# Kernel optimization log

Measured on AMD Instinct MI355X. Metric: run time of the kernel, lower is better.

## Reference

```python
import jax, jax.numpy as jnp
import numpy as np

N = 50000      # nodes
E = 800000     # edges
IN = 64        # in_feats
HID = 4        # hidden_size
OUT = 64       # out_feats
COORS = 3
EPS = 1e-07
NEG_SLOPE = 0.01  # F.leaky_relu default


def setup_inputs() -> dict:
    key = jax.random.key(0)
    ks = jax.random.split(key, 10)
    feat = jax.random.normal(ks[0], (N, IN), dtype=jnp.float32)
    pos = jax.random.normal(ks[1], (N, COORS), dtype=jnp.float32)
    src = jax.random.randint(ks[2], (E,), 0, N, dtype=jnp.int32)
    dst = jax.random.randint(ks[3], (E,), 0, N, dtype=jnp.int32)
    W_self = jax.random.normal(ks[4], (OUT, IN), dtype=jnp.float32) * 0.1
    W_sp = jax.random.normal(ks[5], (HID * IN, COORS), dtype=jnp.float32) * 0.3
    b_sp = jax.random.normal(ks[6], (HID * IN,), dtype=jnp.float32) * 0.05
    W_neigh = jax.random.normal(ks[7], (OUT, HID * IN), dtype=jnp.float32) * 0.05
    b_neigh = jax.random.normal(ks[8], (OUT,), dtype=jnp.float32) * 0.05
    bias = jnp.zeros((OUT,), dtype=jnp.float32)
    return {"feat": feat, "pos": pos, "src": src, "dst": dst,
            "W_self": W_self, "W_sp": W_sp, "b_sp": b_sp,
            "W_neigh": W_neigh, "b_neigh": b_neigh, "bias": bias}


def reference(feat, pos, src, dst, W_self, W_sp, b_sp, W_neigh, b_neigh, bias):
    # per-edge spatial weighting
    rel = pos[dst] - pos[src]                                   # [E, 3]
    scal = jnp.linalg.norm(rel, axis=1, keepdims=True) + EPS    # [E, 1]
    ws = (rel + 1.0) / scal                                     # [E, 3]
    s = jax.nn.leaky_relu(ws @ W_sp.T + b_sp, NEG_SLOPE)        # [E, HID*IN]
    # modulate gathered src features: reshape(E, IN, HID) * h_src[:, :, None]
    msg = (s.reshape(E, IN, HID) * feat[src][:, :, None]).reshape(E, IN * HID)
    # mean aggregation per destination node (zero for isolated nodes)
    neigh_sum = jax.ops.segment_sum(msg, dst, num_segments=N)   # [N, IN*HID]
    cnt = jax.ops.segment_sum(jnp.ones((E,), feat.dtype), dst, num_segments=N)
    neigh_h = neigh_sum / jnp.maximum(cnt, 1.0)[:, None]
    # output projections
    h_neigh = neigh_h @ W_neigh.T + b_neigh                     # [N, OUT]
    rst = feat @ W_self.T + h_neigh + bias                      # [N, OUT]
    return rst
```

## Files before the change

kernel.cpp:

```cpp
#include <hip/hip_runtime.h>
#include <math.h>

#define N_NODES 50000
#define N_EDGES 800000
#define EPS 1e-7f
#define NEG_SLOPE 0.01f

#define SUBCAP 16
#define GSLOTS 64
#define RSTRIDE 72
#define CSTRIDE 16
#define ZPAD 50000u
#define FEAT_BLOCKS (N_NODES * 64 / 4 / 256)
#define EDGE_BLOCKS4 782
#define ACC_STRIDE 264

typedef __attribute__((ext_vector_type(8))) short short8;
typedef __attribute__((ext_vector_type(4))) float f32x4;

__device__ __forceinline__ unsigned bf16_rne(float x) {
    unsigned u = __float_as_uint(x);
    u += 0x7fffu + ((u >> 16) & 1u);
    return u >> 16;
}
__device__ __forceinline__ unsigned pack_bf16(float a, float b) {
    return bf16_rne(a) | (bf16_rne(b) << 16);
}


__global__ __launch_bounds__(256) void pack_hist_kernel(
    const float* __restrict__ feat, uint2* __restrict__ featb2,
    const float* __restrict__ W_neigh, const float* __restrict__ W_self,
    const float* __restrict__ b_neigh, const float* __restrict__ bias,
    unsigned* __restrict__ wnp, unsigned* __restrict__ wsp, float* __restrict__ bb,
    const int* __restrict__ src, const int* __restrict__ dst,
    int* __restrict__ cnt, unsigned short* __restrict__ gsrcs)
{
    const int bid = blockIdx.x;
    if (bid < FEAT_BLOCKS) {
        const int idx = bid * 256 + threadIdx.x;
        float4 v = reinterpret_cast<const float4*>(feat)[idx];
        featb2[idx] = make_uint2(pack_bf16(v.x, v.y), pack_bf16(v.z, v.w));
        return;
    }
    if (bid == FEAT_BLOCKS) {
        const int t = threadIdx.x;
        const float2* Wn2 = (const float2*)W_neigh;
        const float2* Ws2 = (const float2*)W_self;
        for (int i = t; i < 64 * 128; i += 256) {
            float2 v = Wn2[i];
            wnp[i] = pack_bf16(v.x, v.y);
        }
        for (int i = t; i < 64 * 32; i += 256) {
            float2 v = Ws2[i];
            wsp[i] = pack_bf16(v.x, v.y);
        }
        if (t < 64) bb[t] = b_neigh[t] + bias[t];
        if (t < 16) featb2[(size_t)ZPAD * 16 + t] = make_uint2(0u, 0u);
        return;
    }
    const int base = (bid - FEAT_BLOCKS - 1) * 1024 + threadIdx.x * 4;
    if (base >= N_EDGES) return;
    const int4 s4 = *reinterpret_cast<const int4*>(src + base);
    const int4 d4 = *reinterpret_cast<const int4*>(dst + base);
#define EDGE_PUT(S, D, SUB)                                                      \
    {                                                                            \
        const int p = atomicAdd(&cnt[(D) * CSTRIDE + (SUB)], 1);                 \
        if (p < SUBCAP)                                                          \
            __builtin_nontemporal_store(                                         \
                (unsigned short)(S),                                             \
                &gsrcs[(size_t)(D) * GSLOTS + (SUB) * SUBCAP + p]);              \
    }
    EDGE_PUT(s4.x, d4.x, 0)
    EDGE_PUT(s4.y, d4.y, 1)
    EDGE_PUT(s4.z, d4.z, 2)
    EDGE_PUT(s4.w, d4.w, 3)
#undef EDGE_PUT
}


__device__ __forceinline__ float featload(const unsigned short* featb, unsigned rec_y,
                                          int lane) {
    const unsigned idx = ((rec_y >> 10) & 0x3FFFC0u) + (unsigned)lane;
    return __uint_as_float((unsigned)featb[idx] << 16);
}

__global__ __launch_bounds__(256) void aggregate_project_kernel(
    const unsigned short* __restrict__ featb, const float* __restrict__ W_sp,
    const float* __restrict__ b_sp, const int* __restrict__ cnt,
    const unsigned short* __restrict__ gsrcs, const float* __restrict__ pos,
    const short* __restrict__ wnb, const short* __restrict__ wsb,
    const float* __restrict__ bb, float* __restrict__ out)
{
    __shared__ unsigned short accS[16 * ACC_STRIDE];
    __shared__ uint2 recG[16 * RSTRIDE];

    const int lane = threadIdx.x & 63;
    const int w = threadIdx.x >> 6;
    const int nb = blockIdx.x << 4;

    float wsp0[4], wsp1[4], wsp2[4], bsp[4];
#pragma unroll
    for (int h = 0; h < 4; ++h) {
        int j = lane * 4 + h;
        wsp0[h] = W_sp[j * 3 + 0];
        wsp1[h] = W_sp[j * 3 + 1];
        wsp2[h] = W_sp[j * 3 + 2];
        bsp[h]  = b_sp[j];
    }

    const uint2 zrec = make_uint2(0u, ZPAD << 16);
    int dtrue[4], deff[4];
#pragma unroll
    for (int q = 0; q < 4; ++q) {
        const int r = (w << 2) + q;
        const int n = nb + r;
        const int4 c4 = *reinterpret_cast<const int4*>(&cnt[n * CSTRIDE]);
        const int c0 = min(c4.x, SUBCAP), c1 = min(c4.y, SUBCAP),
                  c2 = min(c4.z, SUBCAP), c3 = min(c4.w, SUBCAP);
        dtrue[q] = c4.x + c4.y + c4.z + c4.w;
        const int o1 = c0, o2 = c0 + c1, o3 = o2 + c2;
        deff[q] = o3 + c3;
        recG[r * RSTRIDE + lane] = zrec;
        if (lane < 8) recG[r * RSTRIDE + 64 + lane] = zrec;
        const int sub = lane >> 4, p = lane & 15;
        const int cs = (sub == 0) ? c0 : (sub == 1) ? c1 : (sub == 2) ? c2 : c3;
        const int ob = (sub == 0) ? 0 : (sub == 1) ? o1 : (sub == 2) ? o2 : o3;
        if (p < cs) {
            const int s = (int)gsrcs[(size_t)n * GSLOTS + lane];
            const float rx = pos[n * 3 + 0] - pos[s * 3 + 0];
            const float ry = pos[n * 3 + 1] - pos[s * 3 + 1];
            const float rz = pos[n * 3 + 2] - pos[s * 3 + 2];
            const float inv = __builtin_amdgcn_rcpf(
                __builtin_amdgcn_sqrtf(rx * rx + ry * ry + rz * rz) + EPS);
            const uint2 rec =
                make_uint2(pack_bf16((rx + 1.f) * inv, (ry + 1.f) * inv),
                           bf16_rne((rz + 1.f) * inv) | ((unsigned)s << 16));
            recG[r * RSTRIDE + ob + p] = rec;
        }
    }

#define MLP_ACC(U, F)                                                              \
    {                                                                              \
        const float wx = __uint_as_float((U).x << 16);                             \
        const float wy = __uint_as_float((U).x & 0xffff0000u);                     \
        const float wz = __uint_as_float((U).y << 16);                             \
        float t0 = fmaf(wx, wsp0[0], fmaf(wy, wsp1[0], fmaf(wz, wsp2[0], bsp[0])));\
        float t1 = fmaf(wx, wsp0[1], fmaf(wy, wsp1[1], fmaf(wz, wsp2[1], bsp[1])));\
        float t2 = fmaf(wx, wsp0[2], fmaf(wy, wsp1[2], fmaf(wz, wsp2[2], bsp[2])));\
        float t3 = fmaf(wx, wsp0[3], fmaf(wy, wsp1[3], fmaf(wz, wsp2[3], bsp[3])));\
        a0 = fmaf(fmaxf(t0, t0 * NEG_SLOPE), (F), a0);                             \
        a1 = fmaf(fmaxf(t1, t1 * NEG_SLOPE), (F), a1);                             \
        a2 = fmaf(fmaxf(t2, t2 * NEG_SLOPE), (F), a2);                             \
        a3 = fmaf(fmaxf(t3, t3 * NEG_SLOPE), (F), a3);                             \
    }

#pragma unroll
    for (int q = 0; q < 4; ++q) {
        const int r = (w << 2) + q;
        const int deg = __builtin_amdgcn_readfirstlane(deff[q]);
        const int dt  = __builtin_amdgcn_readfirstlane(dtrue[q]);
        const uint2* gp = &recG[r * RSTRIDE];

        float a0 = 0.f, a1 = 0.f, a2 = 0.f, a3 = 0.f;

        if (deg > 0) {
            uint2 u0 = gp[0], u1 = gp[1], u2 = gp[2], u3 = gp[3];
            float f0 = featload(featb, u0.y, lane);
            float f1 = featload(featb, u1.y, lane);
            float f2 = featload(featb, u2.y, lane);
            float f3 = featload(featb, u3.y, lane);

            for (int e = 0; e < deg; e += 4) {
                uint2 v0 = gp[e + 4], v1 = gp[e + 5];
                uint2 v2 = gp[e + 6], v3 = gp[e + 7];
                float g0 = featload(featb, v0.y, lane);
                float g1 = featload(featb, v1.y, lane);
                float g2 = featload(featb, v2.y, lane);
                float g3 = featload(featb, v3.y, lane);

                MLP_ACC(u0, f0)
                MLP_ACC(u1, f1)
                MLP_ACC(u2, f2)
                MLP_ACC(u3, f3)

                u0 = v0; u1 = v1; u2 = v2; u3 = v3;
                f0 = g0; f1 = g1; f2 = g2; f3 = g3;
            }
        }

        const float mscale = 1.f / fmaxf((float)dt, 1.f);
        uint2 pv = make_uint2(pack_bf16(a0 * mscale, a1 * mscale),
                              pack_bf16(a2 * mscale, a3 * mscale));
        *reinterpret_cast<uint2*>(&accS[r * ACC_STRIDE + lane * 4]) = pv;
    }
#undef MLP_ACC
    __syncthreads();

    const int mrow = lane & 15;
    const int quad = lane >> 4;
    const int o = (w << 4) + mrow;

    f32x4 acc = {0.f, 0.f, 0.f, 0.f};

    const unsigned short* Ar = &accS[mrow * ACC_STRIDE + quad * 8];
    const short* Br = wnb + o * 256 + quad * 8;
#pragma unroll
    for (int ks = 0; ks < 8; ++ks) {
        short8 a = *reinterpret_cast<const short8*>(Ar + ks * 32);
        short8 b = *reinterpret_cast<const short8*>(Br + ks * 32);
        acc = __builtin_amdgcn_mfma_f32_16x16x32_bf16(a, b, acc, 0, 0, 0);
    }

    const short* Fr = (const short*)featb + (size_t)(nb + mrow) * 64 + quad * 8;
    const short* Sr = wsb + o * 64 + quad * 8;
#pragma unroll
    for (int ks = 0; ks < 2; ++ks) {
        short8 a = *reinterpret_cast<const short8*>(Fr + ks * 32);
        short8 b = *reinterpret_cast<const short8*>(Sr + ks * 32);
        acc = __builtin_amdgcn_mfma_f32_16x16x32_bf16(a, b, acc, 0, 0, 0);
    }

    const float badd = bb[o];
#pragma unroll
    for (int r = 0; r < 4; ++r) {
        out[(size_t)(nb + quad * 4 + r) * 64 + o] = acc[r] + badd;
    }
}


extern "C" void kernel_launch(void* const* d_in, const int* in_sizes, int n_in,
                              void* d_out, int out_size, void* d_ws, size_t ws_size,
                              hipStream_t stream) {
    (void)in_sizes; (void)n_in; (void)out_size; (void)ws_size;
    const float* feat    = (const float*)d_in[0];
    const float* pos     = (const float*)d_in[1];
    const int*   src     = (const int*)d_in[2];
    const int*   dst     = (const int*)d_in[3];
    const float* W_self  = (const float*)d_in[4];
    const float* W_sp    = (const float*)d_in[5];
    const float* b_sp    = (const float*)d_in[6];
    const float* W_neigh = (const float*)d_in[7];
    const float* b_neigh = (const float*)d_in[8];
    const float* bias    = (const float*)d_in[9];
    float* out = (float*)d_out;

    unsigned short* gsrcs  = (unsigned short*)d_ws;
    uint2*          featb2 = (uint2*)(gsrcs + (size_t)N_NODES * GSLOTS);
    unsigned int*   wnp    = (unsigned int*)(featb2 + 800016);
    unsigned int*   wsp    = wnp + 8192;
    float*          bb     = (float*)(wsp + 2048);
    int*            cnt    = (int*)(bb + 64);

    hipMemsetAsync(cnt, 0, (size_t)N_NODES * CSTRIDE * sizeof(int), stream);
    pack_hist_kernel<<<FEAT_BLOCKS + 1 + EDGE_BLOCKS4, 256, 0, stream>>>(
        feat, featb2, W_neigh, W_self, b_neigh, bias, wnp, wsp, bb,
        src, dst, cnt, gsrcs);
    aggregate_project_kernel<<<N_NODES / 16, 256, 0, stream>>>(
        (const unsigned short*)featb2, W_sp, b_sp, cnt, gsrcs, pos,
        (const short*)wnp, (const short*)wsp, bb, out);
}
```

Before: 213.1 us.

## Split counter sub-buckets into separate planes and shorten edge loop unroll to two

Each of the four per-node atomic counters now sits in its own plane, one counter per 64-byte slot, so the four sub-bucket atomics for a node go to separate cache lines instead of sharing one. The aggregation loop handles two edges per iteration instead of four, and the second edge's feature is masked to zero when the degree is odd. Because of that masking, padding records can point at node 0 rather than a dedicated zero pad row, so the pad row and its initialisation are removed. The cost is a four times larger counter memset, four scalar counter loads in place of one vector load, and less load-ahead prefetch in the edge loop.

```diff
diff --git a/kernel.cpp b/kernel.cpp
--- a/kernel.cpp
+++ b/kernel.cpp
@@ -10,7 +10,7 @@
 #define GSLOTS 64
 #define RSTRIDE 72
 #define CSTRIDE 16
-#define ZPAD 50000u
+#define CPLANE  (N_NODES * CSTRIDE)
 #define FEAT_BLOCKS (N_NODES * 64 / 4 / 256)
 #define EDGE_BLOCKS4 782
 #define ACC_STRIDE 264
@@ -56,7 +56,6 @@
             wsp[i] = pack_bf16(v.x, v.y);
         }
         if (t < 64) bb[t] = b_neigh[t] + bias[t];
-        if (t < 16) featb2[(size_t)ZPAD * 16 + t] = make_uint2(0u, 0u);
         return;
     }
     const int base = (bid - FEAT_BLOCKS - 1) * 1024 + threadIdx.x * 4;
@@ -65,7 +64,7 @@
     const int4 d4 = *reinterpret_cast<const int4*>(dst + base);
 #define EDGE_PUT(S, D, SUB)                                                      \
     {                                                                            \
-        const int p = atomicAdd(&cnt[(D) * CSTRIDE + (SUB)], 1);                 \
+        const int p = atomicAdd(&cnt[(SUB) * CPLANE + (D) * CSTRIDE], 1);        \
         if (p < SUBCAP)                                                          \
             __builtin_nontemporal_store(                                         \
                 (unsigned short)(S),                                             \
@@ -109,20 +108,23 @@
         bsp[h]  = b_sp[j];
     }
 
-    const uint2 zrec = make_uint2(0u, ZPAD << 16);
     int dtrue[4], deff[4];
 #pragma unroll
     for (int q = 0; q < 4; ++q) {
         const int r = (w << 2) + q;
         const int n = nb + r;
-        const int4 c4 = *reinterpret_cast<const int4*>(&cnt[n * CSTRIDE]);
-        const int c0 = min(c4.x, SUBCAP), c1 = min(c4.y, SUBCAP),
-                  c2 = min(c4.z, SUBCAP), c3 = min(c4.w, SUBCAP);
-        dtrue[q] = c4.x + c4.y + c4.z + c4.w;
+        const int r0 = cnt[0 * CPLANE + n * CSTRIDE];
+        const int r1 = cnt[1 * CPLANE + n * CSTRIDE];
+        const int r2 = cnt[2 * CPLANE + n * CSTRIDE];
+        const int r3 = cnt[3 * CPLANE + n * CSTRIDE];
+        dtrue[q] = r0 + r1 + r2 + r3;
+        const int c0 = min(r0, SUBCAP), c1 = min(r1, SUBCAP),
+                  c2 = min(r2, SUBCAP), c3 = min(r3, SUBCAP);
         const int o1 = c0, o2 = c0 + c1, o3 = o2 + c2;
         deff[q] = o3 + c3;
-        recG[r * RSTRIDE + lane] = zrec;
-        if (lane < 8) recG[r * RSTRIDE + 64 + lane] = zrec;
+        const uint2 z = make_uint2(0u, 0u);
+        recG[r * RSTRIDE + lane] = z;
+        if (lane < 8) recG[r * RSTRIDE + 64 + lane] = z;
         const int sub = lane >> 4, p = lane & 15;
         const int cs = (sub == 0) ? c0 : (sub == 1) ? c1 : (sub == 2) ? c2 : c3;
         const int ob = (sub == 0) ? 0 : (sub == 1) ? o1 : (sub == 2) ? o2 : o3;
@@ -165,27 +167,26 @@
         float a0 = 0.f, a1 = 0.f, a2 = 0.f, a3 = 0.f;
 
         if (deg > 0) {
-            uint2 u0 = gp[0], u1 = gp[1], u2 = gp[2], u3 = gp[3];
+            const int dm = deg - 1;
+            uint2 u0 = gp[0];
+            uint2 u1 = gp[1];
             float f0 = featload(featb, u0.y, lane);
             float f1 = featload(featb, u1.y, lane);
-            float f2 = featload(featb, u2.y, lane);
-            float f3 = featload(featb, u3.y, lane);
-
-            for (int e = 0; e < deg; e += 4) {
-                uint2 v0 = gp[e + 4], v1 = gp[e + 5];
-                uint2 v2 = gp[e + 6], v3 = gp[e + 7];
-                float g0 = featload(featb, v0.y, lane);
-                float g1 = featload(featb, v1.y, lane);
-                float g2 = featload(featb, v2.y, lane);
-                float g3 = featload(featb, v3.y, lane);
+
+            for (int e = 0; e < deg; e += 2) {
+                uint2 u2 = gp[e + 2];
+                uint2 u3 = gp[e + 3];
+                float f2 = featload(featb, u2.y, lane);
+                float f3 = featload(featb, u3.y, lane);
 
                 MLP_ACC(u0, f0)
-                MLP_ACC(u1, f1)
-                MLP_ACC(u2, f2)
-                MLP_ACC(u3, f3)
-
-                u0 = v0; u1 = v1; u2 = v2; u3 = v3;
-                f0 = g0; f1 = g1; f2 = g2; f3 = g3;
+                {
+                    const float fm = (e + 1 <= dm) ? f1 : 0.f;
+                    MLP_ACC(u1, fm)
+                }
+
+                u0 = u2; u1 = u3;
+                f0 = f2; f1 = f3;
             }
         }
 
@@ -247,12 +248,12 @@
 
     unsigned short* gsrcs  = (unsigned short*)d_ws;
     uint2*          featb2 = (uint2*)(gsrcs + (size_t)N_NODES * GSLOTS);
-    unsigned int*   wnp    = (unsigned int*)(featb2 + 800016);
+    unsigned int*   wnp    = (unsigned int*)(featb2 + 800000);
     unsigned int*   wsp    = wnp + 8192;
     float*          bb     = (float*)(wsp + 2048);
     int*            cnt    = (int*)(bb + 64);
 
-    hipMemsetAsync(cnt, 0, (size_t)N_NODES * CSTRIDE * sizeof(int), stream);
+    hipMemsetAsync(cnt, 0, (size_t)4 * CPLANE * sizeof(int), stream);
     pack_hist_kernel<<<FEAT_BLOCKS + 1 + EDGE_BLOCKS4, 256, 0, stream>>>(
         feat, featb2, W_neigh, W_self, b_neigh, bias, wnp, wsp, bb,
         src, dst, cnt, gsrcs);
```

Measured after the change: 199.5 us. 6.4% less time.
